# Kernel optimization log

Measured on AMD Instinct MI355X. Metric: run time of the kernel, lower is better.

Reference implementation:

```python
import jax, jax.numpy as jnp
import numpy as np

B, S, D, HE, HD = 64, 256, 512, 512, 1024  # batch, seq_len, input_dim, hidden_enc, hidden_dec (=2*HE)


def _gru_cell(h, x, Wih, Whh, bih, bhh):
    # single PyTorch-convention GRU step; gate order [r, z, n]
    H = h.shape[-1]
    gi = x @ Wih.T + bih  # [B, 3H]
    gh = h @ Whh.T + bhh
    r = jax.nn.sigmoid(gi[:, :H] + gh[:, :H])
    z = jax.nn.sigmoid(gi[:, H:2 * H] + gh[:, H:2 * H])
    n = jnp.tanh(gi[:, 2 * H:] + r * gh[:, 2 * H:])
    return (1.0 - z) * n + z * h


def _gru_seq(x, Wih, Whh, bih, bhh):
    # x: [B, S, D] -> outputs [B, S, H], zero initial hidden (torch default)
    h0 = jnp.zeros((x.shape[0], Whh.shape[1]), x.dtype)
    def step(h, xt):
        hn = _gru_cell(h, xt, Wih, Whh, bih, bhh)
        return hn, hn
    _, ys = jax.lax.scan(step, h0, jnp.swapaxes(x, 0, 1))
    return jnp.swapaxes(ys, 0, 1)


def _bigru(x, pf, pb):
    fwd = _gru_seq(x, *pf)
    bwd = _gru_seq(x[:, ::-1], *pb)[:, ::-1]
    return jnp.concatenate([fwd, bwd], axis=-1)  # [B, S, 2H]


def setup_inputs() -> dict:
    key = jax.random.key(0)
    ks = iter(jax.random.split(key, 40))
    f = lambda *shape: (jax.random.normal(next(ks), shape, dtype=jnp.float32) * 0.05)
    inp = {
        'input': f(B, 1, S, D),
        'eps': f(B, S, 2 * HE),
    }
    # encoder mu / sigma bidirectional GRUs (forward + backward directions)
    for name in ['mu_f', 'mu_b', 'sg_f', 'sg_b']:
        inp[name + '_Wih'] = f(3 * HE, D)
        inp[name + '_Whh'] = f(3 * HE, HE)
        inp[name + '_bih'] = f(3 * HE)
        inp[name + '_bhh'] = f(3 * HE)
    # decoder GRU (input_dim -> hidden_dec)
    inp['dec_Wih'] = f(3 * HD, D)
    inp['dec_Whh'] = f(3 * HD, HD)
    inp['dec_bih'] = f(3 * HD)
    inp['dec_bhh'] = f(3 * HD)
    # attention Linear(D+HD, 1) and output Linear(HD, D)
    inp['attn_W'] = f(1, D + HD)
    inp['attn_b'] = f(1)
    inp['lin_W'] = f(D, HD)
    inp['lin_b'] = f(D)
    return inp


def reference(input, eps,
              mu_f_Wih, mu_f_Whh, mu_f_bih, mu_f_bhh,
              mu_b_Wih, mu_b_Whh, mu_b_bih, mu_b_bhh,
              sg_f_Wih, sg_f_Whh, sg_f_bih, sg_f_bhh,
              sg_b_Wih, sg_b_Whh, sg_b_bih, sg_b_bhh,
              dec_Wih, dec_Whh, dec_bih, dec_bhh,
              attn_W, attn_b, lin_W, lin_b):
    x = input[:, 0]  # squeeze -> [B, S, D]
    # encoder (dropout is identity at eval)
    mu = _bigru(x, (mu_f_Wih, mu_f_Whh, mu_f_bih, mu_f_bhh),
                   (mu_b_Wih, mu_b_Whh, mu_b_bih, mu_b_bhh))
    logvar = _bigru(x, (sg_f_Wih, sg_f_Whh, sg_f_bih, sg_f_bhh),
                       (sg_b_Wih, sg_b_Whh, sg_b_bih, sg_b_bhh))
    z = mu + eps * jnp.exp(0.5 * logvar)  # [B, S, HD]

    # attention score = Linear([x_t, hidden]); split into precomputed x-part + per-step hidden part
    sx = x @ attn_W[0, :D] + attn_b[0]  # [B, S]
    wah = attn_W[0, D:]                  # [HD]
    pos = jnp.arange(S)

    def step(carry, i):
        hidden, out = carry  # [B, HD], [B, D]
        scores = sx + (hidden @ wah)[:, None]          # [B, S]
        scores = jnp.where(pos[None, :] == i, -jnp.inf, scores)  # leave-one-out
        w = jax.nn.softmax(scores, axis=1)
        ctx = jnp.einsum('bs,bsh->bh', w, z)           # context = decoder init hidden
        h_new = _gru_cell(ctx, out, dec_Wih, dec_Whh, dec_bih, dec_bhh)
        o_new = h_new @ lin_W.T + lin_b
        return (h_new, o_new), o_new

    h0 = jnp.zeros((B, HD), x.dtype)
    o0 = jnp.zeros((B, D), x.dtype)
    _, rec = jax.lax.scan(step, (h0, o0), pos)
    reconstructed = jnp.swapaxes(rec, 0, 1)  # [B, S, D]
    return reconstructed, mu, logvar
```

## Files before the change

### kernel.cpp

```cpp
#include <hip/hip_runtime.h>
#include <hip/hip_bf16.h>

typedef __hip_bfloat16 bf16;
typedef __attribute__((ext_vector_type(8))) short s8v;
typedef __attribute__((ext_vector_type(4))) float f32x4;
typedef __attribute__((ext_vector_type(4))) int int4v;

#define NB 64
#define NS 256
#define ND 512
#define NHE 512
#define NHD 1024
#define NGE 1536
#define NGD 3072

static __device__ __forceinline__ float sigmf(float x){ return 1.0f/(1.0f+__expf(-x)); }
static __device__ __forceinline__ float b2f(unsigned short u){ return __uint_as_float(((unsigned int)u) << 16); }
static __device__ __forceinline__ unsigned short f2bu(float f){
    bf16 v = __float2bfloat16(f);
    return *reinterpret_cast<unsigned short*>(&v);
}
static __device__ __forceinline__ s8v cast8(int4v v){
    union { int4v i; s8v s; } u; u.i = v; return u.s;
}
static __device__ __forceinline__ void st2_llc(const void* p, unsigned int v){
    asm volatile("global_store_short %0, %1, off sc0 sc1"
                 :: "v"((unsigned long long)(uintptr_t)p), "v"(v) : "memory");
}

#define LOADX8(BASEP, A0,A1,A2,A3,A4,A5,A6,A7)                                   \
    asm volatile(                                                                \
        "global_load_dwordx4 %0, %8, off sc0 sc1\n\t"                            \
        "global_load_dwordx4 %1, %8, off offset:64 sc0 sc1\n\t"                  \
        "global_load_dwordx4 %2, %8, off offset:128 sc0 sc1\n\t"                 \
        "global_load_dwordx4 %3, %8, off offset:192 sc0 sc1\n\t"                 \
        "global_load_dwordx4 %4, %8, off offset:256 sc0 sc1\n\t"                 \
        "global_load_dwordx4 %5, %8, off offset:320 sc0 sc1\n\t"                 \
        "global_load_dwordx4 %6, %8, off offset:384 sc0 sc1\n\t"                 \
        "global_load_dwordx4 %7, %8, off offset:448 sc0 sc1\n\t"                 \
        "s_waitcnt vmcnt(0)"                                                     \
        : "=&v"(A0),"=&v"(A1),"=&v"(A2),"=&v"(A3),                               \
          "=&v"(A4),"=&v"(A5),"=&v"(A6),"=&v"(A7)                                \
        : "v"((unsigned long long)(uintptr_t)(BASEP)) : "memory");               \
    __builtin_amdgcn_sched_barrier(0);

static __device__ __forceinline__ void groupbar_flat(unsigned int* base, int step, int nwg){
    __syncthreads();
    if (threadIdx.x == 0){
        unsigned int old = __hip_atomic_fetch_add(base, 1u, __ATOMIC_RELAXED, __HIP_MEMORY_SCOPE_AGENT);
        if ((int)old == step*nwg - 1)
            __hip_atomic_store(base + 32, (unsigned int)step, __ATOMIC_RELAXED, __HIP_MEMORY_SCOPE_AGENT);
        while ((int)__hip_atomic_load(base + 32, __ATOMIC_RELAXED, __HIP_MEMORY_SCOPE_AGENT) < step)
            __builtin_amdgcn_s_sleep(1);
    }
    __syncthreads();
}
static __device__ __forceinline__ void groupbar_tree(unsigned int* base, int step, int leaf){
    __syncthreads();
    if (threadIdx.x == 0){
        unsigned int lo = __hip_atomic_fetch_add(base + leaf*32, 1u, __ATOMIC_RELAXED, __HIP_MEMORY_SCOPE_AGENT);
        if ((int)lo == step*8 - 1){
            unsigned int ro = __hip_atomic_fetch_add(base + 256, 1u, __ATOMIC_RELAXED, __HIP_MEMORY_SCOPE_AGENT);
            if ((int)ro == step*8 - 1)
                __hip_atomic_store(base + 288, (unsigned int)step, __ATOMIC_RELAXED, __HIP_MEMORY_SCOPE_AGENT);
        }
        while ((int)__hip_atomic_load(base + 288, __ATOMIC_RELAXED, __HIP_MEMORY_SCOPE_AGENT) < step)
            __builtin_amdgcn_s_sleep(1);
    }
    __syncthreads();
}

__global__ __launch_bounds__(256) void k_sx(const float* __restrict__ x,
                                            const float* __restrict__ attnW,
                                            const float* __restrict__ attnb,
                                            float* __restrict__ sx){
    int row = blockIdx.x*4 + (threadIdx.x>>6);
    int lane = threadIdx.x & 63;
    float s = 0.f;
    for (int d = lane; d < ND; d += 64) s += x[(size_t)row*ND + d]*attnW[d];
    #pragma unroll
    for (int off = 32; off; off >>= 1) s += __shfl_down(s, off, 64);
    if (lane == 0) sx[row] = s + attnb[0];
}

__global__ __launch_bounds__(256) void k_cvec(const float* __restrict__ dWih,
                                              const float* __restrict__ linb,
                                              const float* __restrict__ dbih,
                                              float* __restrict__ cvec){
    int row = blockIdx.x*4 + (threadIdx.x>>6);
    int lane = threadIdx.x & 63;
    float s = 0.f;
    for (int d = lane; d < ND; d += 64) s += dWih[(size_t)row*ND + d]*linb[d];
    #pragma unroll
    for (int off = 32; off; off >>= 1) s += __shfl_down(s, off, 64);
    if (lane == 0) cvec[row] = s + dbih[row];
}

__global__ __launch_bounds__(256) void k_softprep2(const float* __restrict__ sx,
                                                   float* __restrict__ esb,
                                                   float* __restrict__ Se){
    int b = blockIdx.x, s = threadIdx.x;
    __shared__ float red[256];
    float v = sx[b*NS + s];
    red[s] = v; __syncthreads();
    for (int off = 128; off; off >>= 1){ if (s < off) red[s] = fmaxf(red[s], red[s+off]); __syncthreads(); }
    float mx = red[0]; __syncthreads();
    float ev = __expf(v - mx);
    esb[s*NB + b] = ev;
    red[s] = ev; __syncthreads();
    for (int off = 128; off; off >>= 1){ if (s < off) red[s] += red[s+off]; __syncthreads(); }
    if (s == 0) Se[b] = red[0];
}

__global__ __launch_bounds__(256) void k_cvtW(const float* __restrict__ W, bf16* __restrict__ o){
    size_t i = ((size_t)blockIdx.x*256 + threadIdx.x)*4;
    float4 v = *(const float4*)(W + i);
    o[i+0] = __float2bfloat16(v.x);
    o[i+1] = __float2bfloat16(v.y);
    o[i+2] = __float2bfloat16(v.z);
    o[i+3] = __float2bfloat16(v.w);
}

__global__ __launch_bounds__(256) void k_zexp2(const float* __restrict__ hh,
                                               const float* __restrict__ eps,
                                               bf16* __restrict__ z){
    int t  = blockIdx.x >> 4;
    int hb = blockIdx.x & 15;
    int h0 = hb*64;
    __shared__ float ls[64*69];
    int tid = threadIdx.x;
    #pragma unroll
    for (int q = 0; q < 16; ++q){
        int bb = q*4 + (tid>>6);
        int hc = tid & 63;
        ls[bb*69 + hc] = eps[((size_t)bb*NS + t)*NHD + h0 + hc];
    }
    __syncthreads();
    int b = tid & 63;
    #pragma unroll
    for (int q = 0; q < 16; ++q){
        int hq = q*4 + (tid>>6);
        int h = h0 + hq;
        int dmu = h >> 9;
        int jm  = h & 511;
        float mu = hh[(((size_t)(dmu*NS) + t)*NHE + jm)*NB + b];
        float lv = hh[(((size_t)((2+dmu)*NS) + t)*NHE + jm)*NB + b];
        float ep = ls[b*69 + hq];
        float zv = mu + ep*__expf(0.5f*lv);
        z[((size_t)t*NHD + h)*NB + b] = __float2bfloat16(zv);
    }
}

__global__ __launch_bounds__(256) void k_T2(const bf16* __restrict__ z,
                                            const float* __restrict__ esb,
                                            float* __restrict__ T){
    int h = blockIdx.x;
    int b = threadIdx.x & 63;
    int sq = threadIdx.x >> 6;
    __shared__ float red[4][64];
    float acc = 0.f;
    #pragma unroll 8
    for (int s = sq*64; s < sq*64 + 64; ++s)
        acc += esb[s*NB + b]*__bfloat162float(z[((size_t)s*NHD + h)*NB + b]);
    red[sq][b] = acc; __syncthreads();
    if (sq == 0) T[h*NB + b] = red[0][b] + red[1][b] + red[2][b] + red[3][b];
}

__global__ __launch_bounds__(256) void k_ctx3(const bf16* __restrict__ z,
                                              const float* __restrict__ esb,
                                              const float* __restrict__ Se,
                                              const float* __restrict__ T,
                                              bf16* __restrict__ ctxT,
                                              bf16* __restrict__ ctxB){
    int i  = blockIdx.x >> 4;
    int hb = blockIdx.x & 15;
    int tid = threadIdx.x;
    int b  = tid & 63;
    __shared__ unsigned short tt[64][66];
    float ei  = esb[i*NB + b];
    float inv = 1.0f/(Se[b] - ei);
    #pragma unroll
    for (int q = 0; q < 16; ++q){
        int hl = q*4 + (tid>>6);
        int h = hb*64 + hl;
        float zv = __bfloat162float(z[((size_t)i*NHD + h)*NB + b]);
        float cv = (T[h*NB + b] - ei*zv)*inv;
        unsigned short u = f2bu(cv);
        ctxT[((size_t)i*NHD + h)*NB + b] = *reinterpret_cast<bf16*>(&u);
        tt[hl][b] = u;
    }
    __syncthreads();
    unsigned short* cb = (unsigned short*)ctxB;
    #pragma unroll
    for (int q = 0; q < 16; ++q){
        int bn = q*4 + (tid>>6);
        int hl = tid & 63;
        cb[((size_t)i*NB + bn)*NHD + hb*64 + hl] = tt[hl][bn];
    }
}

__global__ __launch_bounds__(256) void k_outT(const float* __restrict__ hh,
                                              float* __restrict__ outMu,
                                              float* __restrict__ outLv){
    int bx = blockIdx.x;
    int dir = bx >> 11;
    int t  = (bx >> 3) & 255;
    int jb = bx & 7;
    int j0 = jb*64;
    __shared__ float ls[64*65];
    int tid = threadIdx.x;
    #pragma unroll
    for (int q = 0; q < 16; ++q){
        int jj = q*4 + (tid>>6);
        ls[jj*65 + (tid&63)] = hh[(((size_t)dir*NS + t)*NHE + j0 + jj)*NB + (tid&63)];
    }
    __syncthreads();
    float* outp = (dir < 2) ? outMu : outLv;
    int colbase = (dir & 1)*512;
    #pragma unroll
    for (int q = 0; q < 16; ++q){
        int bb = q*4 + (tid>>6);
        int jj = tid & 63;
        outp[((size_t)bb*NS + t)*NHD + colbase + j0 + jj] = ls[jj*65 + bb];
    }
}

__global__ __launch_bounds__(256) void k_gemm_M(
    const float* __restrict__ dWih,
    const float* __restrict__ linW,
    bf16* __restrict__ M){
    int g0 = blockIdx.x*64;
    int h0 = blockIdx.y*64;
    __shared__ float As[64][36];
    __shared__ float Bs[32][68];
    int tid = threadIdx.x, tx = tid & 15, ty = tid >> 4;
    float acc[4][4] = {};
    for (int k0 = 0; k0 < ND; k0 += 32){
        #pragma unroll
        for (int m = 0; m < 8; ++m){
            int idx = m*256 + tid;
            int row = idx >> 5, kk = idx & 31;
            As[row][kk] = dWih[(size_t)(g0+row)*ND + k0 + kk];
            int k2 = idx >> 6, hh2 = idx & 63;
            Bs[k2][hh2] = linW[(size_t)(k0+k2)*NHD + h0 + hh2];
        }
        __syncthreads();
        for (int k = 0; k < 32; ++k){
            float a[4];
            #pragma unroll
            for (int i = 0; i < 4; ++i) a[i] = As[ty*4+i][k];
            float4 b4 = *(const float4*)&Bs[k][tx*4];
            #pragma unroll
            for (int i = 0; i < 4; ++i){
                acc[i][0] += a[i]*b4.x; acc[i][1] += a[i]*b4.y;
                acc[i][2] += a[i]*b4.z; acc[i][3] += a[i]*b4.w;
            }
        }
        __syncthreads();
    }
    #pragma unroll
    for (int i = 0; i < 4; ++i)
        #pragma unroll
        for (int j = 0; j < 4; ++j)
            M[(size_t)(g0+ty*4+i)*NHD + h0 + tx*4 + j] = __float2bfloat16(acc[i][j]);
}

__global__ __launch_bounds__(256, 2) void k_xg_mfma(
    const bf16* __restrict__ xb,
    const bf16* __restrict__ WihB,
    const float* __restrict__ b0, const float* __restrict__ b1,
    const float* __restrict__ b2, const float* __restrict__ b3,
    bf16* __restrict__ Xg){
    int t = blockIdx.x, gblk = blockIdx.y, dir = blockIdx.z;
    const float* bih = dir==0?b0:dir==1?b1:dir==2?b2:b3;
    int tid = threadIdx.x;
    int lane = tid & 63;
    int w = __builtin_amdgcn_readfirstlane(tid >> 6);
    int ln = lane & 15, lk = lane >> 4;
    int g = gblk*64 + w*16 + ln;
    const unsigned short* Bp = (const unsigned short*)WihB + ((size_t)(dir*NGE + g))*512 + lk*8;
    s8v Bf[16];
    #pragma unroll
    for (int q = 0; q < 16; ++q) Bf[q] = *(const s8v*)(Bp + q*32);
    f32x4 C[4] = {};
    const unsigned short* xu = (const unsigned short*)xb;
    #pragma unroll
    for (int m = 0; m < 4; ++m){
        const unsigned short* Ap = xu + ((size_t)(m*16+ln)*NS + t)*ND + lk*8;
        #pragma unroll
        for (int q = 0; q < 16; ++q){
            s8v Af = *(const s8v*)(Ap + q*32);
            C[m] = __builtin_amdgcn_mfma_f32_16x16x32_bf16(Af, Bf[q], C[m], 0, 0, 0);
        }
    }
    float bi = bih[g];
    unsigned short* Op = (unsigned short*)Xg + ((size_t)(dir*NS + t)*NGE + g)*NB;
    #pragma unroll
    for (int m = 0; m < 4; ++m){
        ushort4 o;
        o.x = f2bu(C[m][0] + bi); o.y = f2bu(C[m][1] + bi);
        o.z = f2bu(C[m][2] + bi); o.w = f2bu(C[m][3] + bi);
        *(ushort4*)(Op + m*16 + lk*4) = o;
    }
}

__global__ __launch_bounds__(256, 2) void k_gctx_mfma(
    const bf16* __restrict__ ctxB,
    const bf16* __restrict__ dWhhB,
    const float* __restrict__ bhh,
    bf16* __restrict__ Gctx){
    int i = blockIdx.x, gblk = blockIdx.y;
    int tid = threadIdx.x;
    int lane = tid & 63;
    int w = __builtin_amdgcn_readfirstlane(tid >> 6);
    int ln = lane & 15, lk = lane >> 4;
    int g = gblk*64 + w*16 + ln;
    f32x4 C[4] = {};
    const unsigned short* cu = (const unsigned short*)ctxB;
    const unsigned short* wu = (const unsigned short*)dWhhB;
    #pragma unroll
    for (int kc = 0; kc < 2; ++kc){
        const unsigned short* Bp = wu + (size_t)g*NHD + kc*512 + lk*8;
        s8v Bf[16];
        #pragma unroll
        for (int q = 0; q < 16; ++q) Bf[q] = *(const s8v*)(Bp + q*32);
        #pragma unroll
        for (int m = 0; m < 4; ++m){
            const unsigned short* Ap = cu + ((size_t)i*NB + m*16+ln)*NHD + kc*512 + lk*8;
            #pragma unroll
            for (int q = 0; q < 16; ++q){
                s8v Af = *(const s8v*)(Ap + q*32);
                C[m] = __builtin_amdgcn_mfma_f32_16x16x32_bf16(Af, Bf[q], C[m], 0, 0, 0);
            }
        }
    }
    float bi = bhh[g];
    unsigned short* Op = (unsigned short*)Gctx + ((size_t)i*NGD + g)*NB;
    #pragma unroll
    for (int m = 0; m < 4; ++m){
        ushort4 o;
        o.x = f2bu(C[m][0] + bi); o.y = f2bu(C[m][1] + bi);
        o.z = f2bu(C[m][2] + bi); o.w = f2bu(C[m][3] + bi);
        *(ushort4*)(Op + m*16 + lk*4) = o;
    }
}

__global__ __launch_bounds__(256, 2) void k_rec_mfma(
    const bf16* __restrict__ Ht,
    const bf16* __restrict__ linWB,
    const float* __restrict__ linb,
    float* __restrict__ outRec){
    int i = blockIdx.x, dblk = blockIdx.y;
    int tid = threadIdx.x;
    int lane = tid & 63;
    int w = __builtin_amdgcn_readfirstlane(tid >> 6);
    int ln = lane & 15, lk = lane >> 4;
    int d = dblk*64 + w*16 + ln;
    f32x4 C[4] = {};
    const unsigned short* hu = (const unsigned short*)Ht;
    const unsigned short* wu = (const unsigned short*)linWB;
    #pragma unroll
    for (int kc = 0; kc < 2; ++kc){
        const unsigned short* Bp = wu + (size_t)d*NHD + kc*512 + lk*8;
        s8v Bf[16];
        #pragma unroll
        for (int q = 0; q < 16; ++q) Bf[q] = *(const s8v*)(Bp + q*32);
        #pragma unroll
        for (int m = 0; m < 4; ++m){
            const unsigned short* Ap = hu + ((size_t)i*NB + m*16+ln)*NHD + kc*512 + lk*8;
            #pragma unroll
            for (int q = 0; q < 16; ++q){
                s8v Af = *(const s8v*)(Ap + q*32);
                C[m] = __builtin_amdgcn_mfma_f32_16x16x32_bf16(Af, Bf[q], C[m], 0, 0, 0);
            }
        }
    }
    float lb = linb[d];
    #pragma unroll
    for (int m = 0; m < 4; ++m)
        #pragma unroll
        for (int r = 0; r < 4; ++r){
            int b = m*16 + lk*4 + r;
            outRec[((size_t)b*NS + i)*ND + d] = C[m][r] + lb;
        }
}

__global__ __launch_bounds__(256, 1) void k_enc11(
    const bf16* __restrict__ Xg,
    const bf16* __restrict__ WB,
    const float* __restrict__ b0, const float* __restrict__ b1,
    const float* __restrict__ b2, const float* __restrict__ b3,
    float* __restrict__ hh,
    bf16* __restrict__ hx,
    unsigned int* __restrict__ bar){
    int wg  = blockIdx.x;
    int grp = wg & 15;
    int wl  = wg >> 4;
    int dir = grp >> 2;
    int bq  = grp & 3;
    int tid = threadIdx.x;
    int lane = tid & 63;
    int wid = __builtin_amdgcn_readfirstlane(tid >> 6);
    int jl = wid & 1, kh = wid >> 1;
    int jt = wl*2 + jl;
    int ln = lane & 15, lk = lane >> 4;
    int j  = jt*16 + ln;
    int b0v = bq*16 + lk*4;
    const float* bhh = dir==0?b0:dir==1?b1:dir==2?b2:b3;
    const unsigned short* WBu = (const unsigned short*)WB;
    s8v Bf[3][8];
    #pragma unroll
    for (int g = 0; g < 3; ++g)
        #pragma unroll
        for (int q = 0; q < 8; ++q)
            Bf[g][q] = *(const s8v*)(WBu + ((size_t)(dir*NGE + g*512 + j))*512 + (kh*8+q)*32 + lk*8);
    float br=0.f, bz=0.f, bn=0.f;
    if (kh == 0){ br = bhh[j]; bz = bhh[j+512]; bn = bhh[j+1024]; }
    float hp0=0.f, hp1=0.f, hp2=0.f, hp3=0.f;
    __shared__ float red[2][3][64][4];
    unsigned int* gb = bar + grp*64;
    const unsigned short* Xgu = (const unsigned short*)Xg;
    ushort4 xr, xz, xn;
    if (kh == 0){
        int t0 = (dir & 1) ? 255 : 0;
        size_t xb_ = (size_t)(dir*NS + t0)*NGE;
        xr = *(const ushort4*)(Xgu + (xb_ + j)*NB + b0v);
        xz = *(const ushort4*)(Xgu + (xb_ + j + 512)*NB + b0v);
        xn = *(const ushort4*)(Xgu + (xb_ + j + 1024)*NB + b0v);
    }
    for (int t = 0; t < NS; ++t){
        int tcur = (dir & 1) ? (255 - t) : t;
        f32x4 C0 = {0.f,0.f,0.f,0.f}, C1 = {0.f,0.f,0.f,0.f}, C2 = {0.f,0.f,0.f,0.f};
        if (t > 0){
            const unsigned short* hxr = (const unsigned short*)hx
                + ((size_t)(((t-1)&1)*4 + dir)*64 + bq*16 + ln)*512 + kh*256 + lk*8;
            int4v a0,a1,a2,a3,a4,a5,a6,a7;
            LOADX8(hxr, a0,a1,a2,a3,a4,a5,a6,a7)
            s8v Af;
            #define MF3(AV) Af = cast8(AV); \
                C0 = __builtin_amdgcn_mfma_f32_16x16x32_bf16(Af, Bf[0][__q], C0, 0, 0, 0); \
                C1 = __builtin_amdgcn_mfma_f32_16x16x32_bf16(Af, Bf[1][__q], C1, 0, 0, 0); \
                C2 = __builtin_amdgcn_mfma_f32_16x16x32_bf16(Af, Bf[2][__q], C2, 0, 0, 0);
            { enum {__q=0}; MF3(a0) } { enum {__q=1}; MF3(a1) }
            { enum {__q=2}; MF3(a2) } { enum {__q=3}; MF3(a3) }
            { enum {__q=4}; MF3(a4) } { enum {__q=5}; MF3(a5) }
            { enum {__q=6}; MF3(a6) } { enum {__q=7}; MF3(a7) }
            #undef MF3
        }
        if (kh == 1){
            *(f32x4*)&red[jl][0][lane][0] = C0;
            *(f32x4*)&red[jl][1][lane][0] = C1;
            *(f32x4*)&red[jl][2][lane][0] = C2;
        }
        __syncthreads();
        if (kh == 0){
            C0 += *(const f32x4*)&red[jl][0][lane][0];
            C1 += *(const f32x4*)&red[jl][1][lane][0];
            C2 += *(const f32x4*)&red[jl][2][lane][0];
            {
                float r_ = sigmf(b2f(xr.x) + C0[0] + br);
                float z_ = sigmf(b2f(xz.x) + C1[0] + bz);
                float n_ = tanhf(b2f(xn.x) + r_*(C2[0] + bn));
                hp0 = (1.f - z_)*n_ + z_*hp0;
            }
            {
                float r_ = sigmf(b2f(xr.y) + C0[1] + br);
                float z_ = sigmf(b2f(xz.y) + C1[1] + bz);
                float n_ = tanhf(b2f(xn.y) + r_*(C2[1] + bn));
                hp1 = (1.f - z_)*n_ + z_*hp1;
            }
            {
                float r_ = sigmf(b2f(xr.z) + C0[2] + br);
                float z_ = sigmf(b2f(xz.z) + C1[2] + bz);
                float n_ = tanhf(b2f(xn.z) + r_*(C2[2] + bn));
                hp2 = (1.f - z_)*n_ + z_*hp2;
            }
            {
                float r_ = sigmf(b2f(xr.w) + C0[3] + br);
                float z_ = sigmf(b2f(xz.w) + C1[3] + bz);
                float n_ = tanhf(b2f(xn.w) + r_*(C2[3] + bn));
                hp3 = (1.f - z_)*n_ + z_*hp3;
            }
            f32x4 ho; ho[0] = hp0; ho[1] = hp1; ho[2] = hp2; ho[3] = hp3;
            *(f32x4*)(hh + ((size_t)(dir*NS + tcur)*NHE + j)*NB + b0v) = ho;
            const unsigned short* hw = (const unsigned short*)hx + ((size_t)((t&1)*4 + dir)*64)*512;
            st2_llc(hw + (size_t)(b0v+0)*512 + j, (unsigned int)f2bu(hp0));
            st2_llc(hw + (size_t)(b0v+1)*512 + j, (unsigned int)f2bu(hp1));
            st2_llc(hw + (size_t)(b0v+2)*512 + j, (unsigned int)f2bu(hp2));
            st2_llc(hw + (size_t)(b0v+3)*512 + j, (unsigned int)f2bu(hp3));
            if (t < NS-1){
                int tn = (dir & 1) ? (254 - t) : (t + 1);
                size_t xb_ = (size_t)(dir*NS + tn)*NGE;
                xr = *(const ushort4*)(Xgu + (xb_ + j)*NB + b0v);
                xz = *(const ushort4*)(Xgu + (xb_ + j + 512)*NB + b0v);
                xn = *(const ushort4*)(Xgu + (xb_ + j + 1024)*NB + b0v);
            }
        }
        if (t < NS-1) groupbar_flat(gb, t+1, 16);
    }
}

__global__ __launch_bounds__(256, 1) void k_dec11(
    const bf16* __restrict__ MB,
    const float* __restrict__ cvec,
    const float* __restrict__ dbih,
    const bf16* __restrict__ Gctx,
    const bf16* __restrict__ ctxT,
    float* __restrict__ H,
    bf16* __restrict__ Ht,
    unsigned int* __restrict__ bar){
    int wg  = blockIdx.x;
    int grp = wg & 3;
    int jt  = wg >> 2;
    int tid = threadIdx.x;
    int lane = tid & 63;
    int wid = __builtin_amdgcn_readfirstlane(tid >> 6);
    int ln = lane & 15, lk = lane >> 4;
    int j  = jt*16 + ln;
    int b0v = grp*16 + lk*4;
    const unsigned short* MBu = (const unsigned short*)MB;
    s8v Bf[3][8];
    #pragma unroll
    for (int g = 0; g < 3; ++g)
        #pragma unroll
        for (int q = 0; q < 8; ++q)
            Bf[g][q] = *(const s8v*)(MBu + ((size_t)(g*NHD + j))*NHD + wid*256 + q*32 + lk*8);
    float c0=0.f,c1=0.f,c2=0.f,d0v=0.f,d1v=0.f,d2v=0.f;
    if (wid == 0){
        c0 = cvec[j]; c1 = cvec[j+NHD]; c2 = cvec[j+2*NHD];
        d0v = dbih[j]; d1v = dbih[j+NHD]; d2v = dbih[j+2*NHD];
    }
    __shared__ float red[3][3][64][4];
    unsigned int* gb = bar + grp*512;
    int leaf = jt & 7;
    const unsigned short* Gu = (const unsigned short*)Gctx;
    const unsigned short* Cu = (const unsigned short*)ctxT;
    ushort4 gr, gz, gn, cx;
    if (wid == 0){
        gr = *(const ushort4*)(Gu + (size_t)j*NB + b0v);
        gz = *(const ushort4*)(Gu + (size_t)(j+NHD)*NB + b0v);
        gn = *(const ushort4*)(Gu + (size_t)(j+2*NHD)*NB + b0v);
        cx = *(const ushort4*)(Cu + (size_t)j*NB + b0v);
    }
    for (int i = 0; i < NS; ++i){
        f32x4 C0 = {0.f,0.f,0.f,0.f}, C1 = {0.f,0.f,0.f,0.f}, C2 = {0.f,0.f,0.f,0.f};
        if (i > 0){
            const unsigned short* hxr = (const unsigned short*)Ht
                + ((size_t)(i-1)*NB + grp*16 + ln)*NHD + wid*256 + lk*8;
            int4v a0,a1,a2,a3,a4,a5,a6,a7;
            LOADX8(hxr, a0,a1,a2,a3,a4,a5,a6,a7)
            s8v Af;
            #define MF3(AV) Af = cast8(AV); \
                C0 = __builtin_amdgcn_mfma_f32_16x16x32_bf16(Af, Bf[0][__q], C0, 0, 0, 0); \
                C1 = __builtin_amdgcn_mfma_f32_16x16x32_bf16(Af, Bf[1][__q], C1, 0, 0, 0); \
                C2 = __builtin_amdgcn_mfma_f32_16x16x32_bf16(Af, Bf[2][__q], C2, 0, 0, 0);
            { enum {__q=0}; MF3(a0) } { enum {__q=1}; MF3(a1) }
            { enum {__q=2}; MF3(a2) } { enum {__q=3}; MF3(a3) }
            { enum {__q=4}; MF3(a4) } { enum {__q=5}; MF3(a5) }
            { enum {__q=6}; MF3(a6) } { enum {__q=7}; MF3(a7) }
            #undef MF3
        }
        if (wid != 0){
            *(f32x4*)&red[wid-1][0][lane][0] = C0;
            *(f32x4*)&red[wid-1][1][lane][0] = C1;
            *(f32x4*)&red[wid-1][2][lane][0] = C2;
        }
        __syncthreads();
        if (wid == 0){
            #pragma unroll
            for (int w = 0; w < 3; ++w){
                C0 += *(const f32x4*)&red[w][0][lane][0];
                C1 += *(const f32x4*)&red[w][1][lane][0];
                C2 += *(const f32x4*)&red[w][2][lane][0];
            }
            f32x4 ho;
            {
                float g0v = (i==0) ? d0v : C0[0] + c0;
                float g1v = (i==0) ? d1v : C1[0] + c1;
                float g2v = (i==0) ? d2v : C2[0] + c2;
                float r_ = sigmf(g0v + b2f(gr.x));
                float z_ = sigmf(g1v + b2f(gz.x));
                float n_ = tanhf(g2v + r_*b2f(gn.x));
                ho[0] = (1.f - z_)*n_ + z_*b2f(cx.x);
            }
            {
                float g0v = (i==0) ? d0v : C0[1] + c0;
                float g1v = (i==0) ? d1v : C1[1] + c1;
                float g2v = (i==0) ? d2v : C2[1] + c2;
                float r_ = sigmf(g0v + b2f(gr.y));
                float z_ = sigmf(g1v + b2f(gz.y));
                float n_ = tanhf(g2v + r_*b2f(gn.y));
                ho[1] = (1.f - z_)*n_ + z_*b2f(cx.y);
            }
            {
                float g0v = (i==0) ? d0v : C0[2] + c0;
                float g1v = (i==0) ? d1v : C1[2] + c1;
                float g2v = (i==0) ? d2v : C2[2] + c2;
                float r_ = sigmf(g0v + b2f(gr.z));
                float z_ = sigmf(g1v + b2f(gz.z));
                float n_ = tanhf(g2v + r_*b2f(gn.z));
                ho[2] = (1.f - z_)*n_ + z_*b2f(cx.z);
            }
            {
                float g0v = (i==0) ? d0v : C0[3] + c0;
                float g1v = (i==0) ? d1v : C1[3] + c1;
                float g2v = (i==0) ? d2v : C2[3] + c2;
                float r_ = sigmf(g0v + b2f(gr.w));
                float z_ = sigmf(g1v + b2f(gz.w));
                float n_ = tanhf(g2v + r_*b2f(gn.w));
                ho[3] = (1.f - z_)*n_ + z_*b2f(cx.w);
            }
            *(f32x4*)(H + ((size_t)i*NHD + j)*NB + b0v) = ho;
            const unsigned short* hw = (const unsigned short*)Ht + (size_t)i*NB*NHD;
            st2_llc(hw + (size_t)(b0v+0)*NHD + j, (unsigned int)f2bu(ho[0]));
            st2_llc(hw + (size_t)(b0v+1)*NHD + j, (unsigned int)f2bu(ho[1]));
            st2_llc(hw + (size_t)(b0v+2)*NHD + j, (unsigned int)f2bu(ho[2]));
            st2_llc(hw + (size_t)(b0v+3)*NHD + j, (unsigned int)f2bu(ho[3]));
            if (i < NS-1){
                size_t gbx = (size_t)(i+1)*NGD*NB;
                gr = *(const ushort4*)(Gu + gbx + (size_t)j*NB + b0v);
                gz = *(const ushort4*)(Gu + gbx + (size_t)(j+NHD)*NB + b0v);
                gn = *(const ushort4*)(Gu + gbx + (size_t)(j+2*NHD)*NB + b0v);
                cx = *(const ushort4*)(Cu + ((size_t)(i+1)*NHD + j)*NB + b0v);
            }
        }
        if (i < NS-1) groupbar_tree(gb, i+1, leaf);
    }
}

extern "C" void kernel_launch(void* const* d_in, const int* in_sizes, int n_in,
                              void* d_out, int out_size, void* d_ws, size_t ws_size,
                              hipStream_t stream){
    const float* x   = (const float*)d_in[0];
    const float* eps = (const float*)d_in[1];
    const float* Wih[4]; const float* Whh[4]; const float* bih[4]; const float* bhh[4];
    for (int d = 0; d < 4; ++d){
        Wih[d] = (const float*)d_in[2 + 4*d];
        Whh[d] = (const float*)d_in[3 + 4*d];
        bih[d] = (const float*)d_in[4 + 4*d];
        bhh[d] = (const float*)d_in[5 + 4*d];
    }
    const float* dWih  = (const float*)d_in[18];
    const float* dWhh  = (const float*)d_in[19];
    const float* dbih  = (const float*)d_in[20];
    const float* dbhh  = (const float*)d_in[21];
    const float* attnW = (const float*)d_in[22];
    const float* attnb = (const float*)d_in[23];
    const float* linW  = (const float*)d_in[24];
    const float* linb  = (const float*)d_in[25];

    float* out    = (float*)d_out;
    float* outRec = out;
    float* outMu  = out + 8388608;
    float* outLv  = out + 25165824;

    char* ws = (char*)d_ws;
    bf16*  Xg    = (bf16*)(ws + 0);
    bf16*  Gctx  = (bf16*)(ws + 0);
    float* Hdec  = (float*)(ws + 100663296);
    bf16*  ctxB  = (bf16*)(ws + 167772160);
    float* hh    = (float*)(ws + 201326592);
    bf16*  xb    = (bf16*)(ws + 201326592);
    bf16*  WihB  = (bf16*)(ws + 268435456);
    bf16*  linWB = (bf16*)(ws + 201326592);
    bf16*  dWhhB = (bf16*)(ws + 202375168);
    bf16*  zbuf  = (bf16*)(ws + 335544320);
    bf16*  ctxT  = (bf16*)(ws + 369098752);
    bf16*  MbufB = (bf16*)(ws + 402653184);
    bf16*  WhhB  = (bf16*)(ws + 408944640);
    bf16*  Ht    = (bf16*)(ws + 415236096);
    float* sx    = (float*)(ws + 448790528);
    float* esb   = (float*)(ws + 448856064);
    float* Se    = (float*)(ws + 448921600);
    float* Tbuf  = (float*)(ws + 448925696);
    float* cvec  = (float*)(ws + 449187840);
    unsigned int* barE = (unsigned int*)(ws + 449200128);
    unsigned int* barD = (unsigned int*)(ws + 449216512);
    bf16*  hxb   = (bf16*)(ws + 449232896);

    hipMemsetAsync(ws + 449200128, 0, 32768, stream);

    hipLaunchKernelGGL(k_cvtW, dim3(8192), dim3(256), 0, stream, x, xb);
    for (int d = 0; d < 4; ++d)
        hipLaunchKernelGGL(k_cvtW, dim3(768), dim3(256), 0, stream, Wih[d], WihB + (size_t)d*NGE*NHE);
    for (int d = 0; d < 4; ++d)
        hipLaunchKernelGGL(k_cvtW, dim3(768), dim3(256), 0, stream, Whh[d], WhhB + (size_t)d*NGE*NHE);
    hipLaunchKernelGGL(k_gemm_M, dim3(48,16), dim3(256), 0, stream, dWih, linW, MbufB);
    hipLaunchKernelGGL(k_cvec, dim3(768), dim3(256), 0, stream, dWih, linb, dbih, cvec);
    hipLaunchKernelGGL(k_sx, dim3(4096), dim3(256), 0, stream, x, attnW, attnb, sx);
    hipLaunchKernelGGL(k_softprep2, dim3(64), dim3(256), 0, stream, sx, esb, Se);
    hipLaunchKernelGGL(k_xg_mfma, dim3(256,24,4), dim3(256), 0, stream,
                       xb, WihB, bih[0], bih[1], bih[2], bih[3], Xg);

    {
        void* a[] = { (void*)&Xg, (void*)&WhhB,
                      (void*)&bhh[0], (void*)&bhh[1], (void*)&bhh[2], (void*)&bhh[3],
                      (void*)&hh, (void*)&hxb, (void*)&barE };
        hipLaunchCooperativeKernel((void*)k_enc11, dim3(256), dim3(256), a, 0, stream);
    }

    hipLaunchKernelGGL(k_zexp2, dim3(4096), dim3(256), 0, stream, hh, eps, zbuf);
    hipLaunchKernelGGL(k_outT, dim3(8192), dim3(256), 0, stream, hh, outMu, outLv);
    hipLaunchKernelGGL(k_cvtW, dim3(3072), dim3(256), 0, stream, dWhh, dWhhB);
    hipLaunchKernelGGL(k_cvtW, dim3(512), dim3(256), 0, stream, linW, linWB);
    hipLaunchKernelGGL(k_T2, dim3(1024), dim3(256), 0, stream, zbuf, esb, Tbuf);
    hipLaunchKernelGGL(k_ctx3, dim3(4096), dim3(256), 0, stream, zbuf, esb, Se, Tbuf, ctxT, ctxB);
    hipLaunchKernelGGL(k_gctx_mfma, dim3(256,48), dim3(256), 0, stream, ctxB, dWhhB, dbhh, Gctx);

    {
        void* a[] = { (void*)&MbufB, (void*)&cvec, (void*)&dbih, (void*)&Gctx, (void*)&ctxT,
                      (void*)&Hdec, (void*)&Ht, (void*)&barD };
        hipLaunchCooperativeKernel((void*)k_dec11, dim3(256), dim3(256), a, 0, stream);
    }

    hipLaunchKernelGGL(k_rec_mfma, dim3(256,8), dim3(256), 0, stream, Ht, linWB, linb, outRec);
}
```

Before: 3.949 ms.

## Replace atomic counter barriers with per-workgroup flags and drop fp32 hidden stores

```diff
diff --git a/kernel.cpp b/kernel.cpp
--- a/kernel.cpp
+++ b/kernel.cpp
@@ -44,32 +44,6 @@
         : "v"((unsigned long long)(uintptr_t)(BASEP)) : "memory");               \
     __builtin_amdgcn_sched_barrier(0);
 
-static __device__ __forceinline__ void groupbar_flat(unsigned int* base, int step, int nwg){
-    __syncthreads();
-    if (threadIdx.x == 0){
-        unsigned int old = __hip_atomic_fetch_add(base, 1u, __ATOMIC_RELAXED, __HIP_MEMORY_SCOPE_AGENT);
-        if ((int)old == step*nwg - 1)
-            __hip_atomic_store(base + 32, (unsigned int)step, __ATOMIC_RELAXED, __HIP_MEMORY_SCOPE_AGENT);
-        while ((int)__hip_atomic_load(base + 32, __ATOMIC_RELAXED, __HIP_MEMORY_SCOPE_AGENT) < step)
-            __builtin_amdgcn_s_sleep(1);
-    }
-    __syncthreads();
-}
-static __device__ __forceinline__ void groupbar_tree(unsigned int* base, int step, int leaf){
-    __syncthreads();
-    if (threadIdx.x == 0){
-        unsigned int lo = __hip_atomic_fetch_add(base + leaf*32, 1u, __ATOMIC_RELAXED, __HIP_MEMORY_SCOPE_AGENT);
-        if ((int)lo == step*8 - 1){
-            unsigned int ro = __hip_atomic_fetch_add(base + 256, 1u, __ATOMIC_RELAXED, __HIP_MEMORY_SCOPE_AGENT);
-            if ((int)ro == step*8 - 1)
-                __hip_atomic_store(base + 288, (unsigned int)step, __ATOMIC_RELAXED, __HIP_MEMORY_SCOPE_AGENT);
-        }
-        while ((int)__hip_atomic_load(base + 288, __ATOMIC_RELAXED, __HIP_MEMORY_SCOPE_AGENT) < step)
-            __builtin_amdgcn_s_sleep(1);
-    }
-    __syncthreads();
-}
-
 __global__ __launch_bounds__(256) void k_sx(const float* __restrict__ x,
                                             const float* __restrict__ attnW,
                                             const float* __restrict__ attnb,
@@ -121,33 +95,56 @@
     o[i+3] = __float2bfloat16(v.w);
 }
 
-__global__ __launch_bounds__(256) void k_zexp2(const float* __restrict__ hh,
+__global__ __launch_bounds__(256) void k_zexp3(const bf16* __restrict__ hxh,
                                                const float* __restrict__ eps,
                                                bf16* __restrict__ z){
     int t  = blockIdx.x >> 4;
     int hb = blockIdx.x & 15;
-    int h0 = hb*64;
-    __shared__ float ls[64*69];
+    int dmu = hb >> 3;
+    int jm0 = (hb & 7)*64;
+    const unsigned short* hu = (const unsigned short*)hxh;
+    __shared__ unsigned short zt[64][66];
     int tid = threadIdx.x;
     #pragma unroll
     for (int q = 0; q < 16; ++q){
         int bb = q*4 + (tid>>6);
         int hc = tid & 63;
-        ls[bb*69 + hc] = eps[((size_t)bb*NS + t)*NHD + h0 + hc];
+        float mu = b2f(hu[(((size_t)(dmu*NS) + t)*64 + bb)*512 + jm0 + hc]);
+        float lv = b2f(hu[(((size_t)((2+dmu)*NS) + t)*64 + bb)*512 + jm0 + hc]);
+        float ep = eps[((size_t)bb*NS + t)*NHD + hb*64 + hc];
+        zt[bb][hc] = f2bu(mu + ep*__expf(0.5f*lv));
     }
     __syncthreads();
+    unsigned short* zu = (unsigned short*)z;
     int b = tid & 63;
     #pragma unroll
     for (int q = 0; q < 16; ++q){
-        int hq = q*4 + (tid>>6);
-        int h = h0 + hq;
-        int dmu = h >> 9;
-        int jm  = h & 511;
-        float mu = hh[(((size_t)(dmu*NS) + t)*NHE + jm)*NB + b];
-        float lv = hh[(((size_t)((2+dmu)*NS) + t)*NHE + jm)*NB + b];
-        float ep = ls[b*69 + hq];
-        float zv = mu + ep*__expf(0.5f*lv);
-        z[((size_t)t*NHD + h)*NB + b] = __float2bfloat16(zv);
+        int hl = q*4 + (tid>>6);
+        zu[((size_t)t*NHD + hb*64 + hl)*NB + b] = zt[b][hl];
+    }
+}
+
+__global__ __launch_bounds__(256) void k_outT2(const bf16* __restrict__ hxh,
+                                               float* __restrict__ outMu,
+                                               float* __restrict__ outLv){
+    int t  = blockIdx.x;
+    int b0 = blockIdx.y*8;
+    const unsigned short* hu = (const unsigned short*)hxh;
+    int tid = threadIdx.x;
+    #pragma unroll
+    for (int q = 0; q < 16; ++q){
+        int idx = q*256 + tid;
+        int sel = idx >> 11;
+        int rem = idx & 2047;
+        int bb  = b0 + (rem >> 8);
+        int h   = (rem & 255)*4;
+        int dirn = (h >> 9) + sel*2;
+        int j   = h & 511;
+        ushort4 v = *(const ushort4*)(hu + (((size_t)(dirn*NS) + t)*64 + bb)*512 + j);
+        float4 o;
+        o.x = b2f(v.x); o.y = b2f(v.y); o.z = b2f(v.z); o.w = b2f(v.w);
+        float* outp = sel ? outLv : outMu;
+        *(float4*)(outp + ((size_t)bb*NS + t)*NHD + h) = o;
     }
 }
 
@@ -196,32 +193,6 @@
         int bn = q*4 + (tid>>6);
         int hl = tid & 63;
         cb[((size_t)i*NB + bn)*NHD + hb*64 + hl] = tt[hl][bn];
-    }
-}
-
-__global__ __launch_bounds__(256) void k_outT(const float* __restrict__ hh,
-                                              float* __restrict__ outMu,
-                                              float* __restrict__ outLv){
-    int bx = blockIdx.x;
-    int dir = bx >> 11;
-    int t  = (bx >> 3) & 255;
-    int jb = bx & 7;
-    int j0 = jb*64;
-    __shared__ float ls[64*65];
-    int tid = threadIdx.x;
-    #pragma unroll
-    for (int q = 0; q < 16; ++q){
-        int jj = q*4 + (tid>>6);
-        ls[jj*65 + (tid&63)] = hh[(((size_t)dir*NS + t)*NHE + j0 + jj)*NB + (tid&63)];
-    }
-    __syncthreads();
-    float* outp = (dir < 2) ? outMu : outLv;
-    int colbase = (dir & 1)*512;
-    #pragma unroll
-    for (int q = 0; q < 16; ++q){
-        int bb = q*4 + (tid>>6);
-        int jj = tid & 63;
-        outp[((size_t)bb*NS + t)*NHD + colbase + j0 + jj] = ls[jj*65 + bb];
     }
 }
 
@@ -385,14 +356,13 @@
         }
 }
 
-__global__ __launch_bounds__(256, 1) void k_enc11(
+__global__ __launch_bounds__(256, 1) void k_enc12(
     const bf16* __restrict__ Xg,
     const bf16* __restrict__ WB,
     const float* __restrict__ b0, const float* __restrict__ b1,
     const float* __restrict__ b2, const float* __restrict__ b3,
-    float* __restrict__ hh,
-    bf16* __restrict__ hx,
-    unsigned int* __restrict__ bar){
+    bf16* __restrict__ hxh,
+    unsigned int* __restrict__ flagE){
     int wg  = blockIdx.x;
     int grp = wg & 15;
     int wl  = wg >> 4;
@@ -418,8 +388,9 @@
     if (kh == 0){ br = bhh[j]; bz = bhh[j+512]; bn = bhh[j+1024]; }
     float hp0=0.f, hp1=0.f, hp2=0.f, hp3=0.f;
     __shared__ float red[2][3][64][4];
-    unsigned int* gb = bar + grp*64;
+    unsigned int* fg = flagE + grp*16;
     const unsigned short* Xgu = (const unsigned short*)Xg;
+    const unsigned short* hu = (const unsigned short*)hxh;
     ushort4 xr, xz, xn;
     if (kh == 0){
         int t0 = (dir & 1) ? 255 : 0;
@@ -432,8 +403,9 @@
         int tcur = (dir & 1) ? (255 - t) : t;
         f32x4 C0 = {0.f,0.f,0.f,0.f}, C1 = {0.f,0.f,0.f,0.f}, C2 = {0.f,0.f,0.f,0.f};
         if (t > 0){
-            const unsigned short* hxr = (const unsigned short*)hx
-                + ((size_t)(((t-1)&1)*4 + dir)*64 + bq*16 + ln)*512 + kh*256 + lk*8;
+            int tprev = (dir & 1) ? (256 - t) : (t - 1);
+            const unsigned short* hxr = hu
+                + (((size_t)(dir*NS + tprev))*64 + bq*16 + ln)*512 + kh*256 + lk*8;
             int4v a0,a1,a2,a3,a4,a5,a6,a7;
             LOADX8(hxr, a0,a1,a2,a3,a4,a5,a6,a7)
             s8v Af;
@@ -481,9 +453,7 @@
                 float n_ = tanhf(b2f(xn.w) + r_*(C2[3] + bn));
                 hp3 = (1.f - z_)*n_ + z_*hp3;
             }
-            f32x4 ho; ho[0] = hp0; ho[1] = hp1; ho[2] = hp2; ho[3] = hp3;
-            *(f32x4*)(hh + ((size_t)(dir*NS + tcur)*NHE + j)*NB + b0v) = ho;
-            const unsigned short* hw = (const unsigned short*)hx + ((size_t)((t&1)*4 + dir)*64)*512;
+            const unsigned short* hw = hu + ((size_t)(dir*NS + tcur))*64*512;
             st2_llc(hw + (size_t)(b0v+0)*512 + j, (unsigned int)f2bu(hp0));
             st2_llc(hw + (size_t)(b0v+1)*512 + j, (unsigned int)f2bu(hp1));
             st2_llc(hw + (size_t)(b0v+2)*512 + j, (unsigned int)f2bu(hp2));
@@ -496,19 +466,28 @@
                 xn = *(const ushort4*)(Xgu + (xb_ + j + 1024)*NB + b0v);
             }
         }
-        if (t < NS-1) groupbar_flat(gb, t+1, 16);
-    }
-}
-
-__global__ __launch_bounds__(256, 1) void k_dec11(
+        __syncthreads();
+        if (t < NS-1){
+            if (tid == 0)
+                __hip_atomic_store(fg + wl, (unsigned int)(t+1), __ATOMIC_RELAXED, __HIP_MEMORY_SCOPE_AGENT);
+            if (wid == 0){
+                int src = lane & 15;
+                while (!__all((int)__hip_atomic_load(fg + src, __ATOMIC_RELAXED, __HIP_MEMORY_SCOPE_AGENT) >= t+1))
+                    __builtin_amdgcn_s_sleep(1);
+            }
+            __syncthreads();
+        }
+    }
+}
+
+__global__ __launch_bounds__(256, 1) void k_dec12(
     const bf16* __restrict__ MB,
     const float* __restrict__ cvec,
     const float* __restrict__ dbih,
     const bf16* __restrict__ Gctx,
     const bf16* __restrict__ ctxT,
-    float* __restrict__ H,
     bf16* __restrict__ Ht,
-    unsigned int* __restrict__ bar){
+    unsigned int* __restrict__ flagD){
     int wg  = blockIdx.x;
     int grp = wg & 3;
     int jt  = wg >> 2;
@@ -531,10 +510,10 @@
         d0v = dbih[j]; d1v = dbih[j+NHD]; d2v = dbih[j+2*NHD];
     }
     __shared__ float red[3][3][64][4];
-    unsigned int* gb = bar + grp*512;
-    int leaf = jt & 7;
+    unsigned int* fg = flagD + grp*64;
     const unsigned short* Gu = (const unsigned short*)Gctx;
     const unsigned short* Cu = (const unsigned short*)ctxT;
+    const unsigned short* hu = (const unsigned short*)Ht;
     ushort4 gr, gz, gn, cx;
     if (wid == 0){
         gr = *(const ushort4*)(Gu + (size_t)j*NB + b0v);
@@ -545,7 +524,7 @@
     for (int i = 0; i < NS; ++i){
         f32x4 C0 = {0.f,0.f,0.f,0.f}, C1 = {0.f,0.f,0.f,0.f}, C2 = {0.f,0.f,0.f,0.f};
         if (i > 0){
-            const unsigned short* hxr = (const unsigned short*)Ht
+            const unsigned short* hxr = hu
                 + ((size_t)(i-1)*NB + grp*16 + ln)*NHD + wid*256 + lk*8;
             int4v a0,a1,a2,a3,a4,a5,a6,a7;
             LOADX8(hxr, a0,a1,a2,a3,a4,a5,a6,a7)
@@ -610,8 +589,7 @@
                 float n_ = tanhf(g2v + r_*b2f(gn.w));
                 ho[3] = (1.f - z_)*n_ + z_*b2f(cx.w);
             }
-            *(f32x4*)(H + ((size_t)i*NHD + j)*NB + b0v) = ho;
-            const unsigned short* hw = (const unsigned short*)Ht + (size_t)i*NB*NHD;
+            const unsigned short* hw = hu + (size_t)i*NB*NHD;
             st2_llc(hw + (size_t)(b0v+0)*NHD + j, (unsigned int)f2bu(ho[0]));
             st2_llc(hw + (size_t)(b0v+1)*NHD + j, (unsigned int)f2bu(ho[1]));
             st2_llc(hw + (size_t)(b0v+2)*NHD + j, (unsigned int)f2bu(ho[2]));
@@ -624,7 +602,16 @@
                 cx = *(const ushort4*)(Cu + ((size_t)(i+1)*NHD + j)*NB + b0v);
             }
         }
-        if (i < NS-1) groupbar_tree(gb, i+1, leaf);
+        __syncthreads();
+        if (i < NS-1){
+            if (tid == 0)
+                __hip_atomic_store(fg + jt, (unsigned int)(i+1), __ATOMIC_RELAXED, __HIP_MEMORY_SCOPE_AGENT);
+            if (wid == 0){
+                while (!__all((int)__hip_atomic_load(fg + lane, __ATOMIC_RELAXED, __HIP_MEMORY_SCOPE_AGENT) >= i+1))
+                    __builtin_amdgcn_s_sleep(1);
+            }
+            __syncthreads();
+        }
     }
 }
 
@@ -657,28 +644,26 @@
     char* ws = (char*)d_ws;
     bf16*  Xg    = (bf16*)(ws + 0);
     bf16*  Gctx  = (bf16*)(ws + 0);
-    float* Hdec  = (float*)(ws + 100663296);
-    bf16*  ctxB  = (bf16*)(ws + 167772160);
-    float* hh    = (float*)(ws + 201326592);
-    bf16*  xb    = (bf16*)(ws + 201326592);
-    bf16*  WihB  = (bf16*)(ws + 268435456);
-    bf16*  linWB = (bf16*)(ws + 201326592);
-    bf16*  dWhhB = (bf16*)(ws + 202375168);
-    bf16*  zbuf  = (bf16*)(ws + 335544320);
-    bf16*  ctxT  = (bf16*)(ws + 369098752);
-    bf16*  MbufB = (bf16*)(ws + 402653184);
-    bf16*  WhhB  = (bf16*)(ws + 408944640);
-    bf16*  Ht    = (bf16*)(ws + 415236096);
-    float* sx    = (float*)(ws + 448790528);
-    float* esb   = (float*)(ws + 448856064);
-    float* Se    = (float*)(ws + 448921600);
-    float* Tbuf  = (float*)(ws + 448925696);
-    float* cvec  = (float*)(ws + 449187840);
-    unsigned int* barE = (unsigned int*)(ws + 449200128);
-    unsigned int* barD = (unsigned int*)(ws + 449216512);
-    bf16*  hxb   = (bf16*)(ws + 449232896);
-
-    hipMemsetAsync(ws + 449200128, 0, 32768, stream);
+    bf16*  ctxB  = (bf16*)(ws + 100663296);
+    bf16*  hxh   = (bf16*)(ws + 201326592);
+    bf16*  zbuf  = (bf16*)(ws + 268435456);
+    bf16*  ctxT  = (bf16*)(ws + 301989888);
+    bf16*  Ht    = (bf16*)(ws + 335544320);
+    bf16*  xb    = (bf16*)(ws + 369098752);
+    bf16*  WihB  = (bf16*)(ws + 385875968);
+    bf16*  WhhB  = (bf16*)(ws + 392167424);
+    bf16*  MbufB = (bf16*)(ws + 398458880);
+    bf16*  dWhhB = (bf16*)(ws + 404750336);
+    bf16*  linWB = (bf16*)(ws + 411041792);
+    float* sx    = (float*)(ws + 412090368);
+    float* esb   = (float*)(ws + 412155904);
+    float* Se    = (float*)(ws + 412221440);
+    float* Tbuf  = (float*)(ws + 412225536);
+    float* cvec  = (float*)(ws + 412487680);
+    unsigned int* flagE = (unsigned int*)(ws + 412499968);
+    unsigned int* flagD = (unsigned int*)(ws + 412500992);
+
+    hipMemsetAsync(ws + 412499968, 0, 8192, stream);
 
     hipLaunchKernelGGL(k_cvtW, dim3(8192), dim3(256), 0, stream, x, xb);
     for (int d = 0; d < 4; ++d)
@@ -695,12 +680,12 @@
     {
         void* a[] = { (void*)&Xg, (void*)&WhhB,
                       (void*)&bhh[0], (void*)&bhh[1], (void*)&bhh[2], (void*)&bhh[3],
-                      (void*)&hh, (void*)&hxb, (void*)&barE };
-        hipLaunchCooperativeKernel((void*)k_enc11, dim3(256), dim3(256), a, 0, stream);
-    }
-
-    hipLaunchKernelGGL(k_zexp2, dim3(4096), dim3(256), 0, stream, hh, eps, zbuf);
-    hipLaunchKernelGGL(k_outT, dim3(8192), dim3(256), 0, stream, hh, outMu, outLv);
+                      (void*)&hxh, (void*)&flagE };
+        hipLaunchCooperativeKernel((void*)k_enc12, dim3(256), dim3(256), a, 0, stream);
+    }
+
+    hipLaunchKernelGGL(k_zexp3, dim3(4096), dim3(256), 0, stream, hxh, eps, zbuf);
+    hipLaunchKernelGGL(k_outT2, dim3(256,8), dim3(256), 0, stream, hxh, outMu, outLv);
     hipLaunchKernelGGL(k_cvtW, dim3(3072), dim3(256), 0, stream, dWhh, dWhhB);
     hipLaunchKernelGGL(k_cvtW, dim3(512), dim3(256), 0, stream, linW, linWB);
     hipLaunchKernelGGL(k_T2, dim3(1024), dim3(256), 0, stream, zbuf, esb, Tbuf);
@@ -709,8 +694,8 @@
 
     {
         void* a[] = { (void*)&MbufB, (void*)&cvec, (void*)&dbih, (void*)&Gctx, (void*)&ctxT,
-                      (void*)&Hdec, (void*)&Ht, (void*)&barD };
-        hipLaunchCooperativeKernel((void*)k_dec11, dim3(256), dim3(256), a, 0, stream);
+                      (void*)&Ht, (void*)&flagD };
+        hipLaunchCooperativeKernel((void*)k_dec12, dim3(256), dim3(256), a, 0, stream);
     }
 
     hipLaunchKernelGGL(k_rec_mfma, dim3(256,8), dim3(256), 0, stream, Ht, linWB, linb, outRec);
```

Measured after the change: 4.301 ms. 1.09x slower.
